# Kernel optimization log

Measured on AMD Instinct MI355X. Metric: run time of the kernel, lower is better.

The kernel has to match this reference:

```python
import jax, jax.numpy as jnp
import numpy as np

B, L, E, S = 4, 1024, 256, 32  # batch, seq_len, e_dim, local window half-size
NEG = -1e30  # stands in for excluding out-of-range positions from softmax


def setup_inputs() -> dict:
    key = jax.random.key(0)
    ks = jax.random.split(key, 8)
    sc = 1.0 / np.sqrt(E)
    return {
        "q": jax.random.normal(ks[0], (B, L, E), jnp.float32),
        "Wq": jax.random.normal(ks[1], (E, E), jnp.float32) * sc,
        "bq": jax.random.normal(ks[2], (E,), jnp.float32) * sc,
        "Wk": jax.random.normal(ks[3], (E, E), jnp.float32) * sc,
        "bk": jax.random.normal(ks[4], (E,), jnp.float32) * sc,
        "Wv": jax.random.normal(ks[5], (E, E), jnp.float32) * sc,
        "bv": jax.random.normal(ks[6], (E,), jnp.float32) * sc,
        "pos_bias": jax.random.normal(ks[7], (2 * S + 1, E), jnp.float32),
    }


def reference(q, Wq, bq, Wk, bk, Wv, bv, pos_bias):
    # Linear projections (nn.Linear: x @ W.T + b)
    Q = q @ Wq.T + bq
    K = q @ Wk.T + bk
    V = q @ Wv.T + bv

    W = 2 * S + 1
    rel = jnp.arange(-S, S + 1)                      # [W] relative offsets
    idx = jnp.arange(L)[:, None] + rel[None, :]       # [L, W] absolute positions
    valid = (idx >= 0) & (idx < L)                    # in-sequence window entries
    idxc = jnp.clip(idx, 0, L - 1)
    strict = jnp.abs(rel) < S                         # |j-i| < s mask (zeroes K at edges)

    # Gather windows: [B, L, W, E]
    K_win = K[:, idxc] + pos_bias[rel + S][None, None, :, :]
    K_masked = jnp.where(strict[None, None, :, None], K_win, 0.0)
    # Out-of-range positions excluded from softmax entirely (logit -> -inf)
    logits = jnp.where(valid[None, :, :, None], Q[:, :, None, :] * K_masked, NEG)
    weights = jax.nn.softmax(logits, axis=2)          # per-channel softmax over window

    V_win = jnp.where(valid[None, :, :, None], V[:, idxc], 0.0)
    ctx = jnp.sum(weights * V_win, axis=2)            # [B, L, E]

    sig = jax.nn.sigmoid(Q)
    # sigmoid applied inside the loop and again at the end -> squared
    return sig * sig * ctx
```

## Files before the change

kernel.cpp:

```cpp
#include <hip/hip_runtime.h>
#include <hip/hip_bf16.h>

#define B_ 4
#define L_ 1024
#define E_ 256
#define S_ 32

typedef __bf16 bf16x8 __attribute__((ext_vector_type(8)));
typedef float f32x4 __attribute__((ext_vector_type(4)));

__device__ __forceinline__ __bf16 bf_from_bits(unsigned short u) {
    __bf16 b;
    __builtin_memcpy(&b, &u, 2);
    return b;
}

__device__ __forceinline__ void split1(float x, unsigned short& h, unsigned short& l) {
    const unsigned u  = __float_as_uint(x);
    const unsigned hb = u & 0xFFFF0000u;
    h = (unsigned short)(hb >> 16);
    __bf16 lo = (__bf16)(x - __uint_as_float(hb));
    unsigned short lu;
    __builtin_memcpy(&lu, &lo, 2);
    l = lu;
}

__device__ __forceinline__ void load8split(const float* __restrict__ p,
                                           bf16x8& h, bf16x8& l) {
    const float4 x0 = *(const float4*)p;
    const float4 x1 = *(const float4*)(p + 4);
    const float xs[8] = {x0.x, x0.y, x0.z, x0.w, x1.x, x1.y, x1.z, x1.w};
#pragma unroll
    for (int j = 0; j < 8; ++j) {
        const unsigned hb = __float_as_uint(xs[j]) & 0xFFFF0000u;
        h[j] = bf_from_bits((unsigned short)(__float_as_uint(xs[j]) >> 16));
        l[j] = (__bf16)(xs[j] - __uint_as_float(hb));
    }
}

__global__ __launch_bounds__(256) void presplit(
    const float* __restrict__ A,
    const float* __restrict__ Wq, const float* __restrict__ Wk,
    const float* __restrict__ Wv,
    unsigned short* __restrict__ Ah, unsigned short* __restrict__ Al,
    unsigned short* __restrict__ Wh, unsigned short* __restrict__ Wl)
{
    const int e8 = (blockIdx.x * 256 + threadIdx.x) * 8;
    const float* src;
    unsigned short* dh;
    unsigned short* dl;
    if (e8 < 1048576) {
        src = A + e8; dh = Ah + e8; dl = Al + e8;
    } else {
        const int r = e8 - 1048576;
        const int m = r >> 16;
        const int o = r & 65535;
        src = (m == 0 ? Wq : m == 1 ? Wk : Wv) + o;
        dh = Wh + r; dl = Wl + r;
    }
    const float4 x0 = *(const float4*)src;
    const float4 x1 = *(const float4*)(src + 4);
    const float xs[8] = {x0.x, x0.y, x0.z, x0.w, x1.x, x1.y, x1.z, x1.w};
    unsigned short hs[8], ls[8];
#pragma unroll
    for (int j = 0; j < 8; ++j) split1(xs[j], hs[j], ls[j]);
    *(ushort4*)(dh)     = make_ushort4(hs[0], hs[1], hs[2], hs[3]);
    *(ushort4*)(dh + 4) = make_ushort4(hs[4], hs[5], hs[6], hs[7]);
    *(ushort4*)(dl)     = make_ushort4(ls[0], ls[1], ls[2], ls[3]);
    *(ushort4*)(dl + 4) = make_ushort4(ls[4], ls[5], ls[6], ls[7]);
}

__global__ __launch_bounds__(256, 2) void qkv_gemm3(
    const unsigned short* __restrict__ Ah, const unsigned short* __restrict__ Al,
    const unsigned short* __restrict__ Wh, const unsigned short* __restrict__ Wl,
    const float* __restrict__ bq, const float* __restrict__ bk,
    const float* __restrict__ bv,
    float* __restrict__ Qo, float* __restrict__ Ko, float* __restrict__ Vo)
{
    const int z = blockIdx.z;
    const float* bm = (z == 0) ? bq : (z == 1) ? bk : bv;
    float* Om       = (z == 0) ? Qo : (z == 1) ? Ko : Vo;
    const unsigned short* Whz = Wh + (size_t)z * 65536;
    const unsigned short* Wlz = Wl + (size_t)z * 65536;

    const int wave = threadIdx.x >> 6;
    const int lane = threadIdx.x & 63;
    const int rsel = lane & 15;
    const int koff = (lane >> 4) * 8;

    const int m0 = blockIdx.x * 32;
    const int nb = wave * 64;

    const unsigned short* pa0h = Ah + (size_t)(m0 + rsel) * 256 + koff;
    const unsigned short* pa0l = Al + (size_t)(m0 + rsel) * 256 + koff;
    const unsigned short* pa1h = pa0h + 16 * 256;
    const unsigned short* pa1l = pa0l + 16 * 256;

    const unsigned short* pwh[4];
    const unsigned short* pwl[4];
#pragma unroll
    for (int nt = 0; nt < 4; ++nt) {
        const size_t off = (size_t)(nb + nt * 16 + rsel) * 256 + koff;
        pwh[nt] = Whz + off;
        pwl[nt] = Wlz + off;
    }

    f32x4 acc[2][4];
#pragma unroll
    for (int mt = 0; mt < 2; ++mt)
#pragma unroll
        for (int nt = 0; nt < 4; ++nt)
            acc[mt][nt] = (f32x4){0.f, 0.f, 0.f, 0.f};

#pragma unroll
    for (int k0 = 0; k0 < 256; k0 += 32) {
        bf16x8 ah[2], al[2], bh[4], bl[4];
        ah[0] = *(const bf16x8*)(pa0h + k0);
        al[0] = *(const bf16x8*)(pa0l + k0);
        ah[1] = *(const bf16x8*)(pa1h + k0);
        al[1] = *(const bf16x8*)(pa1l + k0);
#pragma unroll
        for (int nt = 0; nt < 4; ++nt) {
            bh[nt] = *(const bf16x8*)(pwh[nt] + k0);
            bl[nt] = *(const bf16x8*)(pwl[nt] + k0);
        }
#pragma unroll
        for (int mt = 0; mt < 2; ++mt)
#pragma unroll
            for (int nt = 0; nt < 4; ++nt) {
                acc[mt][nt] = __builtin_amdgcn_mfma_f32_16x16x32_bf16(
                    ah[mt], bh[nt], acc[mt][nt], 0, 0, 0);
                acc[mt][nt] = __builtin_amdgcn_mfma_f32_16x16x32_bf16(
                    ah[mt], bl[nt], acc[mt][nt], 0, 0, 0);
                acc[mt][nt] = __builtin_amdgcn_mfma_f32_16x16x32_bf16(
                    al[mt], bh[nt], acc[mt][nt], 0, 0, 0);
            }
    }

#pragma unroll
    for (int mt = 0; mt < 2; ++mt) {
        const int mrow = m0 + mt * 16 + (lane >> 4) * 4;
#pragma unroll
        for (int nt = 0; nt < 4; ++nt) {
            const int n = nb + nt * 16 + rsel;
            const float bias = bm[n];
#pragma unroll
            for (int r = 0; r < 4; ++r)
                Om[(size_t)(mrow + r) * 256 + n] = acc[mt][nt][r] + bias;
        }
    }
}

#define TI2 32
#define CH2 64
#define HB2 96
#define PS2 68
#define LOG2E 1.4426950408889634f

__global__ __launch_bounds__(256) void aft_stage2c(
    const float* __restrict__ Q, const float* __restrict__ K,
    const float* __restrict__ V, const float* __restrict__ pb,
    float* __restrict__ out)
{
    __shared__ float Kw[HB2][PS2];
    __shared__ float Vw[HB2][PS2];
    __shared__ float Pw[2 * S_ + 1][PS2];

    const int tid = threadIdx.x;
    const int b  = blockIdx.y;
    const int i0 = blockIdx.x * TI2;
    const int c0 = blockIdx.z * CH2;

    const float* Kb = K + (size_t)b * L_ * E_;
    const float* Vb = V + (size_t)b * L_ * E_;

    for (int idx = tid; idx < HB2 * 16; idx += 256) {
        const int r  = idx >> 4;
        const int cq = (idx & 15) * 4;
        int j = i0 - S_ + r;
        j = j < 0 ? 0 : (j > L_ - 1 ? L_ - 1 : j);
        const size_t g = (size_t)j * E_ + c0 + cq;
        *(float4*)&Kw[r][cq] = *(const float4*)(Kb + g);
        *(float4*)&Vw[r][cq] = *(const float4*)(Vb + g);
    }
    for (int idx = tid; idx < (2 * S_ + 1) * 16; idx += 256) {
        const int r  = idx >> 4;
        const int cq = (idx & 15) * 4;
        *(float4*)&Pw[r][cq] = *(const float4*)(pb + (size_t)r * E_ + c0 + cq);
    }
    __syncthreads();

    const int cq = (tid & 15) * 4;
    const int t  = tid >> 4;
    const int i1 = i0 + 2 * t;
    const int i2 = i1 + 1;
    const int r0 = 2 * t;

    const float4 qa = *(const float4*)(Q + ((size_t)b * L_ + i1) * E_ + c0 + cq);
    const float4 qb2 = *(const float4*)(Q + ((size_t)b * L_ + i2) * E_ + c0 + cq);
    const float4 q2a = make_float4(qa.x * LOG2E, qa.y * LOG2E, qa.z * LOG2E, qa.w * LOG2E);
    const float4 q2b = make_float4(qb2.x * LOG2E, qb2.y * LOG2E, qb2.z * LOG2E, qb2.w * LOG2E);

    float4 den1 = {0, 0, 0, 0}, num1 = {0, 0, 0, 0};
    float4 den2 = {0, 0, 0, 0}, num2 = {0, 0, 0, 0};

    const bool interior = (blockIdx.x >= 1) && (blockIdx.x <= (L_ / TI2) - 2);

    if (interior) {
        {
            const float4 v = *(const float4*)&Vw[r0][cq];
            den1.x += 1.f; den1.y += 1.f; den1.z += 1.f; den1.w += 1.f;
            num1.x += v.x; num1.y += v.y; num1.z += v.z; num1.w += v.w;
        }
        float4 p_old;
        {
            const float4 p = *(const float4*)&Pw[1][cq];
            const float4 k = *(const float4*)&Kw[r0 + 1][cq];
            const float4 v = *(const float4*)&Vw[r0 + 1][cq];
            const float e0 = __builtin_amdgcn_exp2f(q2a.x * (k.x + p.x));
            const float e1 = __builtin_amdgcn_exp2f(q2a.y * (k.y + p.y));
            const float e2 = __builtin_amdgcn_exp2f(q2a.z * (k.z + p.z));
            const float e3 = __builtin_amdgcn_exp2f(q2a.w * (k.w + p.w));
            den1.x += e0; den1.y += e1; den1.z += e2; den1.w += e3;
            num1.x += e0 * v.x; num1.y += e1 * v.y; num1.z += e2 * v.z; num1.w += e3 * v.w;
            den2.x += 1.f; den2.y += 1.f; den2.z += 1.f; den2.w += 1.f;
            num2.x += v.x; num2.y += v.y; num2.z += v.z; num2.w += v.w;
            p_old = p;
        }
        for (int w1 = 2; w1 <= 63; ++w1) {
            const float4 p = *(const float4*)&Pw[w1][cq];
            const float4 k = *(const float4*)&Kw[r0 + w1][cq];
            const float4 v = *(const float4*)&Vw[r0 + w1][cq];
            const float a0 = __builtin_amdgcn_exp2f(q2a.x * (k.x + p.x));
            const float a1 = __builtin_amdgcn_exp2f(q2a.y * (k.y + p.y));
            const float a2 = __builtin_amdgcn_exp2f(q2a.z * (k.z + p.z));
            const float a3 = __builtin_amdgcn_exp2f(q2a.w * (k.w + p.w));
            const float b0 = __builtin_amdgcn_exp2f(q2b.x * (k.x + p_old.x));
            const float b1 = __builtin_amdgcn_exp2f(q2b.y * (k.y + p_old.y));
            const float b2 = __builtin_amdgcn_exp2f(q2b.z * (k.z + p_old.z));
            const float b3 = __builtin_amdgcn_exp2f(q2b.w * (k.w + p_old.w));
            den1.x += a0; den1.y += a1; den1.z += a2; den1.w += a3;
            num1.x += a0 * v.x; num1.y += a1 * v.y; num1.z += a2 * v.z; num1.w += a3 * v.w;
            den2.x += b0; den2.y += b1; den2.z += b2; den2.w += b3;
            num2.x += b0 * v.x; num2.y += b1 * v.y; num2.z += b2 * v.z; num2.w += b3 * v.w;
            p_old = p;
        }
        {
            const float4 k = *(const float4*)&Kw[r0 + 64][cq];
            const float4 v = *(const float4*)&Vw[r0 + 64][cq];
            den1.x += 1.f; den1.y += 1.f; den1.z += 1.f; den1.w += 1.f;
            num1.x += v.x; num1.y += v.y; num1.z += v.z; num1.w += v.w;
            const float b0 = __builtin_amdgcn_exp2f(q2b.x * (k.x + p_old.x));
            const float b1 = __builtin_amdgcn_exp2f(q2b.y * (k.y + p_old.y));
            const float b2 = __builtin_amdgcn_exp2f(q2b.z * (k.z + p_old.z));
            const float b3 = __builtin_amdgcn_exp2f(q2b.w * (k.w + p_old.w));
            den2.x += b0; den2.y += b1; den2.z += b2; den2.w += b3;
            num2.x += b0 * v.x; num2.y += b1 * v.y; num2.z += b2 * v.z; num2.w += b3 * v.w;
        }
        {
            const float4 v = *(const float4*)&Vw[r0 + 65][cq];
            den2.x += 1.f; den2.y += 1.f; den2.z += 1.f; den2.w += 1.f;
            num2.x += v.x; num2.y += v.y; num2.z += v.z; num2.w += v.w;
        }
    } else {
#pragma unroll
        for (int rowsel = 0; rowsel < 2; ++rowsel) {
            const int i = rowsel ? i2 : i1;
            const float4 q2 = rowsel ? q2b : q2a;
            float4* den = rowsel ? &den2 : &den1;
            float4* num = rowsel ? &num2 : &num1;
            for (int w = 0; w <= 64; ++w) {
                const int j = i - S_ + w;
                const bool valid = (unsigned)j < (unsigned)L_;
                const int r = (i - i0) + w;
                const float4 k = *(const float4*)&Kw[r][cq];
                const float4 v = *(const float4*)&Vw[r][cq];
                const float4 p = *(const float4*)&Pw[w][cq];
                const bool edge = (w == 0) || (w == 64);
                const float lx = edge ? 0.f : q2.x * (k.x + p.x);
                const float ly = edge ? 0.f : q2.y * (k.y + p.y);
                const float lz = edge ? 0.f : q2.z * (k.z + p.z);
                const float lw = edge ? 0.f : q2.w * (k.w + p.w);
                const float e0 = valid ? __builtin_amdgcn_exp2f(lx) : 0.f;
                const float e1 = valid ? __builtin_amdgcn_exp2f(ly) : 0.f;
                const float e2 = valid ? __builtin_amdgcn_exp2f(lz) : 0.f;
                const float e3 = valid ? __builtin_amdgcn_exp2f(lw) : 0.f;
                den->x += e0; den->y += e1; den->z += e2; den->w += e3;
                num->x += e0 * v.x; num->y += e1 * v.y;
                num->z += e2 * v.z; num->w += e3 * v.w;
            }
        }
    }

    {
        const float s0 = 1.f / (1.f + __builtin_amdgcn_exp2f(-q2a.x));
        const float s1 = 1.f / (1.f + __builtin_amdgcn_exp2f(-q2a.y));
        const float s2 = 1.f / (1.f + __builtin_amdgcn_exp2f(-q2a.z));
        const float s3 = 1.f / (1.f + __builtin_amdgcn_exp2f(-q2a.w));
        float4 o;
        o.x = s0 * s0 * num1.x / den1.x;
        o.y = s1 * s1 * num1.y / den1.y;
        o.z = s2 * s2 * num1.z / den1.z;
        o.w = s3 * s3 * num1.w / den1.w;
        *(float4*)(out + ((size_t)b * L_ + i1) * E_ + c0 + cq) = o;
    }
    {
        const float s0 = 1.f / (1.f + __builtin_amdgcn_exp2f(-q2b.x));
        const float s1 = 1.f / (1.f + __builtin_amdgcn_exp2f(-q2b.y));
        const float s2 = 1.f / (1.f + __builtin_amdgcn_exp2f(-q2b.z));
        const float s3 = 1.f / (1.f + __builtin_amdgcn_exp2f(-q2b.w));
        float4 o;
        o.x = s0 * s0 * num2.x / den2.x;
        o.y = s1 * s1 * num2.y / den2.y;
        o.z = s2 * s2 * num2.z / den2.z;
        o.w = s3 * s3 * num2.w / den2.w;
        *(float4*)(out + ((size_t)b * L_ + i2) * E_ + c0 + cq) = o;
    }
}

#define TI 32
#define CG 64
#define RK 96
#define LDP 68

__global__ __launch_bounds__(256) void aft_fused(
    const float* __restrict__ q,
    const float* __restrict__ Wq, const float* __restrict__ bq,
    const float* __restrict__ Wk, const float* __restrict__ bk,
    const float* __restrict__ Wv, const float* __restrict__ bv,
    const float* __restrict__ pb,
    float* __restrict__ out)
{
    __shared__ float Kl[RK][LDP];
    __shared__ float Vl[RK][LDP];
    __shared__ float Ql[TI][LDP];

    const int i0 = blockIdx.x * TI;
    const int b  = blockIdx.y;
    const int c0 = blockIdx.z * CG;

    const int wave = threadIdx.x >> 6;
    const int lane = threadIdx.x & 63;
    const int rsel = lane & 15;
    const int koff = (lane >> 4) * 8;

    const float* qb = q + (size_t)b * L_ * E_;

    for (int job = wave; job < 56; job += 4) {
        int p, rt, ct;
        if (job < 24)      { p = 0; rt = job >> 2;        ct = job & 3; }
        else if (job < 48) { p = 1; rt = (job - 24) >> 2; ct = (job - 24) & 3; }
        else               { p = 2; rt = (job - 48) >> 2; ct = (job - 48) & 3; }

        int jrow = (p == 2) ? (i0 + rt * 16 + rsel)
                            : (i0 - S_ + rt * 16 + rsel);
        int jc = jrow < 0 ? 0 : (jrow > L_ - 1 ? L_ - 1 : jrow);
        const float* pa = qb + (size_t)jc * E_ + koff;

        const float* Wm = (p == 0) ? Wk : (p == 1) ? Wv : Wq;
        const float* bm = (p == 0) ? bk : (p == 1) ? bv : bq;
        const int n = c0 + ct * 16 + rsel;
        const float* pw = Wm + (size_t)n * E_ + koff;

        f32x4 acc = {0.f, 0.f, 0.f, 0.f};
#pragma unroll
        for (int k0 = 0; k0 < 256; k0 += 32) {
            bf16x8 ah, al, bh, bl;
            load8split(pa + k0, ah, al);
            load8split(pw + k0, bh, bl);
            acc = __builtin_amdgcn_mfma_f32_16x16x32_bf16(ah, bh, acc, 0, 0, 0);
            acc = __builtin_amdgcn_mfma_f32_16x16x32_bf16(ah, bl, acc, 0, 0, 0);
            acc = __builtin_amdgcn_mfma_f32_16x16x32_bf16(al, bh, acc, 0, 0, 0);
        }

        const float bias = bm[n];
        const int row0 = rt * 16 + (lane >> 4) * 4;
        const int colc = ct * 16 + rsel;
        float* dst = (p == 0) ? &Kl[0][0] : (p == 1) ? &Vl[0][0] : &Ql[0][0];
#pragma unroll
        for (int r = 0; r < 4; ++r)
            dst[(size_t)(row0 + r) * LDP + colc] = acc[r] + bias;
    }
    __syncthreads();

    const int cq  = threadIdx.x & 15;
    const int is0 = threadIdx.x >> 4;
    const int cL  = cq * 4;
    const int cG  = c0 + cL;
    const float* pbc = pb + cG;

    for (int rr = is0; rr < TI; rr += 16) {
        const int i = i0 + rr;
        const float4 qv = *(const float4*)&Ql[rr][cL];

        float den0 = 0.f, den1 = 0.f, den2 = 0.f, den3 = 0.f;
        float num0 = 0.f, num1 = 0.f, num2 = 0.f, num3 = 0.f;

        const int jlo = (i - S_ < 0) ? 0 : (i - S_);
        const int jhi = (i + S_ > L_ - 1) ? (L_ - 1) : (i + S_);

        for (int j = jlo; j <= jhi; ++j) {
            const int r = j - (i0 - S_);
            const int w = j - i + S_;
            const float4 vv = *(const float4*)&Vl[r][cL];

            float kx = 0.f, ky = 0.f, kz = 0.f, kw = 0.f;
            if (w != 0 && w != 2 * S_) {
                const float4 kk = *(const float4*)&Kl[r][cL];
                const float4 pp = *(const float4*)(pbc + (size_t)w * E_);
                kx = kk.x + pp.x;
                ky = kk.y + pp.y;
                kz = kk.z + pp.z;
                kw = kk.w + pp.w;
            }
            const float e0 = __expf(qv.x * kx);
            const float e1 = __expf(qv.y * ky);
            const float e2 = __expf(qv.z * kz);
            const float e3 = __expf(qv.w * kw);
            den0 += e0; den1 += e1; den2 += e2; den3 += e3;
            num0 += e0 * vv.x; num1 += e1 * vv.y;
            num2 += e2 * vv.z; num3 += e3 * vv.w;
        }

        const float s0 = 1.f / (1.f + __expf(-qv.x));
        const float s1 = 1.f / (1.f + __expf(-qv.y));
        const float s2 = 1.f / (1.f + __expf(-qv.z));
        const float s3 = 1.f / (1.f + __expf(-qv.w));

        float4 o;
        o.x = s0 * s0 * num0 / den0;
        o.y = s1 * s1 * num1 / den1;
        o.z = s2 * s2 * num2 / den2;
        o.w = s3 * s3 * num3 / den3;
        *(float4*)(out + ((size_t)b * L_ + i) * E_ + cG) = o;
    }
}

extern "C" void kernel_launch(void* const* d_in, const int* in_sizes, int n_in,
                              void* d_out, int out_size, void* d_ws, size_t ws_size,
                              hipStream_t stream) {
    const float* q  = (const float*)d_in[0];
    const float* Wq = (const float*)d_in[1];
    const float* bq = (const float*)d_in[2];
    const float* Wk = (const float*)d_in[3];
    const float* bk = (const float*)d_in[4];
    const float* Wv = (const float*)d_in[5];
    const float* bv = (const float*)d_in[6];
    const float* pb = (const float*)d_in[7];

    const size_t needA = (size_t)3 * 1048576 * 4 + (size_t)2 * 1048576 * 2
                       + (size_t)2 * 196608 * 2;

    if (ws_size >= needA) {
        float* Qf = (float*)d_ws;
        float* Kf = Qf + 1048576;
        float* Vf = Kf + 1048576;
        unsigned short* Ah = (unsigned short*)(Vf + 1048576);
        unsigned short* Al = Ah + 1048576;
        unsigned short* Wh = Al + 1048576;
        unsigned short* Wl = Wh + 196608;

        presplit<<<dim3(608), 256, 0, stream>>>(q, Wq, Wk, Wv, Ah, Al, Wh, Wl);
        qkv_gemm3<<<dim3(128, 1, 3), 256, 0, stream>>>(Ah, Al, Wh, Wl,
                                                       bq, bk, bv, Qf, Kf, Vf);
        aft_stage2c<<<dim3(L_ / TI2, B_, E_ / CH2), 256, 0, stream>>>(
            Qf, Kf, Vf, pb, (float*)d_out);
    } else {
        aft_fused<<<dim3(L_ / TI, B_, E_ / CG), 256, 0, stream>>>(
            q, Wq, bq, Wk, bk, Wv, bv, pb, (float*)d_out);
    }
}
```

Baseline: 126.7 us.

## Fuse QKV projection GEMM into local-window attention kernel via shared memory

Result: slower. 145.5 us (+14.9%).

```diff
diff --git a/kernel.cpp b/kernel.cpp
--- a/kernel.cpp
+++ b/kernel.cpp
@@ -70,123 +70,81 @@
     *(ushort4*)(dl + 4) = make_ushort4(ls[4], ls[5], ls[6], ls[7]);
 }
 
-__global__ __launch_bounds__(256, 2) void qkv_gemm3(
+#define PS2 68
+#define LOG2E 1.4426950408889634f
+
+__global__ __launch_bounds__(256, 2) void aft_fused2(
     const unsigned short* __restrict__ Ah, const unsigned short* __restrict__ Al,
     const unsigned short* __restrict__ Wh, const unsigned short* __restrict__ Wl,
     const float* __restrict__ bq, const float* __restrict__ bk,
-    const float* __restrict__ bv,
-    float* __restrict__ Qo, float* __restrict__ Ko, float* __restrict__ Vo)
+    const float* __restrict__ bv, const float* __restrict__ pb,
+    float* __restrict__ out)
 {
-    const int z = blockIdx.z;
-    const float* bm = (z == 0) ? bq : (z == 1) ? bk : bv;
-    float* Om       = (z == 0) ? Qo : (z == 1) ? Ko : Vo;
-    const unsigned short* Whz = Wh + (size_t)z * 65536;
-    const unsigned short* Wlz = Wl + (size_t)z * 65536;
-
-    const int wave = threadIdx.x >> 6;
-    const int lane = threadIdx.x & 63;
+    __shared__ float Kw[96][PS2];
+    __shared__ float Vw[96][PS2];
+    __shared__ float Qw[32][PS2];
+    __shared__ float Pw[2 * S_ + 1][PS2];
+
+    const int tid = threadIdx.x;
+    const int i0 = blockIdx.x * 32;
+    const int b  = blockIdx.y;
+    const int c0 = blockIdx.z * 64;
+
+    for (int idx = tid; idx < (2 * S_ + 1) * 16; idx += 256) {
+        const int r  = idx >> 4;
+        const int cc = (idx & 15) * 4;
+        *(float4*)&Pw[r][cc] = *(const float4*)(pb + (size_t)r * E_ + c0 + cc);
+    }
+
+    const int wave = tid >> 6;
+    const int lane = tid & 63;
     const int rsel = lane & 15;
     const int koff = (lane >> 4) * 8;
 
-    const int m0 = blockIdx.x * 32;
-    const int nb = wave * 64;
-
-    const unsigned short* pa0h = Ah + (size_t)(m0 + rsel) * 256 + koff;
-    const unsigned short* pa0l = Al + (size_t)(m0 + rsel) * 256 + koff;
-    const unsigned short* pa1h = pa0h + 16 * 256;
-    const unsigned short* pa1l = pa0l + 16 * 256;
-
-    const unsigned short* pwh[4];
-    const unsigned short* pwl[4];
-#pragma unroll
-    for (int nt = 0; nt < 4; ++nt) {
-        const size_t off = (size_t)(nb + nt * 16 + rsel) * 256 + koff;
-        pwh[nt] = Whz + off;
-        pwl[nt] = Wlz + off;
-    }
-
-    f32x4 acc[2][4];
-#pragma unroll
-    for (int mt = 0; mt < 2; ++mt)
-#pragma unroll
-        for (int nt = 0; nt < 4; ++nt)
-            acc[mt][nt] = (f32x4){0.f, 0.f, 0.f, 0.f};
-
-#pragma unroll
-    for (int k0 = 0; k0 < 256; k0 += 32) {
-        bf16x8 ah[2], al[2], bh[4], bl[4];
-        ah[0] = *(const bf16x8*)(pa0h + k0);
-        al[0] = *(const bf16x8*)(pa0l + k0);
-        ah[1] = *(const bf16x8*)(pa1h + k0);
-        al[1] = *(const bf16x8*)(pa1l + k0);
-#pragma unroll
-        for (int nt = 0; nt < 4; ++nt) {
-            bh[nt] = *(const bf16x8*)(pwh[nt] + k0);
-            bl[nt] = *(const bf16x8*)(pwl[nt] + k0);
-        }
-#pragma unroll
-        for (int mt = 0; mt < 2; ++mt)
-#pragma unroll
-            for (int nt = 0; nt < 4; ++nt) {
-                acc[mt][nt] = __builtin_amdgcn_mfma_f32_16x16x32_bf16(
-                    ah[mt], bh[nt], acc[mt][nt], 0, 0, 0);
-                acc[mt][nt] = __builtin_amdgcn_mfma_f32_16x16x32_bf16(
-                    ah[mt], bl[nt], acc[mt][nt], 0, 0, 0);
-                acc[mt][nt] = __builtin_amdgcn_mfma_f32_16x16x32_bf16(
-                    al[mt], bh[nt], acc[mt][nt], 0, 0, 0);
+    const int ct = wave;
+    const int n  = c0 + ct * 16 + rsel;
+    const int colc = ct * 16 + rsel;
+    const int crow = (lane >> 4) * 4;
+
+#pragma unroll
+    for (int p = 0; p < 3; ++p) {
+        const int z = (p == 0) ? 1 : (p == 1) ? 2 : 0;
+        const float bias = (p == 0) ? bk[n] : (p == 1) ? bv[n] : bq[n];
+        float* dst = (p == 0) ? &Kw[0][0] : (p == 1) ? &Vw[0][0] : &Qw[0][0];
+        const int nrt = (p == 2) ? 2 : 6;
+
+        const unsigned short* wh = Wh + (size_t)z * 65536 + (size_t)n * 256 + koff;
+        const unsigned short* wl = Wl + (size_t)z * 65536 + (size_t)n * 256 + koff;
+        bf16x8 BH[8], BL[8];
+#pragma unroll
+        for (int s = 0; s < 8; ++s) {
+            BH[s] = *(const bf16x8*)(wh + s * 32);
+            BL[s] = *(const bf16x8*)(wl + s * 32);
+        }
+
+        for (int rt = 0; rt < nrt; ++rt) {
+            int arow = (p == 2) ? (i0 + rt * 16 + rsel)
+                                : (i0 - S_ + rt * 16 + rsel);
+            arow = arow < 0 ? 0 : (arow > L_ - 1 ? L_ - 1 : arow);
+            const size_t abase = ((size_t)b * L_ + arow) * 256 + koff;
+            const unsigned short* pah = Ah + abase;
+            const unsigned short* pal = Al + abase;
+
+            f32x4 acc = {0.f, 0.f, 0.f, 0.f};
+#pragma unroll
+            for (int s = 0; s < 8; ++s) {
+                const bf16x8 ah = *(const bf16x8*)(pah + s * 32);
+                const bf16x8 al = *(const bf16x8*)(pal + s * 32);
+                acc = __builtin_amdgcn_mfma_f32_16x16x32_bf16(ah, BH[s], acc, 0, 0, 0);
+                acc = __builtin_amdgcn_mfma_f32_16x16x32_bf16(ah, BL[s], acc, 0, 0, 0);
+                acc = __builtin_amdgcn_mfma_f32_16x16x32_bf16(al, BH[s], acc, 0, 0, 0);
             }
-    }
-
-#pragma unroll
-    for (int mt = 0; mt < 2; ++mt) {
-        const int mrow = m0 + mt * 16 + (lane >> 4) * 4;
-#pragma unroll
-        for (int nt = 0; nt < 4; ++nt) {
-            const int n = nb + nt * 16 + rsel;
-            const float bias = bm[n];
+
+            const int row0 = rt * 16 + crow;
 #pragma unroll
             for (int r = 0; r < 4; ++r)
-                Om[(size_t)(mrow + r) * 256 + n] = acc[mt][nt][r] + bias;
-        }
-    }
-}
-
-#define TI2 32
-#define CH2 64
-#define HB2 96
-#define PS2 68
-#define LOG2E 1.4426950408889634f
-
-__global__ __launch_bounds__(256) void aft_stage2c(
-    const float* __restrict__ Q, const float* __restrict__ K,
-    const float* __restrict__ V, const float* __restrict__ pb,
-    float* __restrict__ out)
-{
-    __shared__ float Kw[HB2][PS2];
-    __shared__ float Vw[HB2][PS2];
-    __shared__ float Pw[2 * S_ + 1][PS2];
-
-    const int tid = threadIdx.x;
-    const int b  = blockIdx.y;
-    const int i0 = blockIdx.x * TI2;
-    const int c0 = blockIdx.z * CH2;
-
-    const float* Kb = K + (size_t)b * L_ * E_;
-    const float* Vb = V + (size_t)b * L_ * E_;
-
-    for (int idx = tid; idx < HB2 * 16; idx += 256) {
-        const int r  = idx >> 4;
-        const int cq = (idx & 15) * 4;
-        int j = i0 - S_ + r;
-        j = j < 0 ? 0 : (j > L_ - 1 ? L_ - 1 : j);
-        const size_t g = (size_t)j * E_ + c0 + cq;
-        *(float4*)&Kw[r][cq] = *(const float4*)(Kb + g);
-        *(float4*)&Vw[r][cq] = *(const float4*)(Vb + g);
-    }
-    for (int idx = tid; idx < (2 * S_ + 1) * 16; idx += 256) {
-        const int r  = idx >> 4;
-        const int cq = (idx & 15) * 4;
-        *(float4*)&Pw[r][cq] = *(const float4*)(pb + (size_t)r * E_ + c0 + cq);
+                dst[(size_t)(row0 + r) * PS2 + colc] = acc[r] + bias;
+        }
     }
     __syncthreads();
 
@@ -196,15 +154,15 @@
     const int i2 = i1 + 1;
     const int r0 = 2 * t;
 
-    const float4 qa = *(const float4*)(Q + ((size_t)b * L_ + i1) * E_ + c0 + cq);
-    const float4 qb2 = *(const float4*)(Q + ((size_t)b * L_ + i2) * E_ + c0 + cq);
+    const float4 qa  = *(const float4*)&Qw[2 * t][cq];
+    const float4 qb2 = *(const float4*)&Qw[2 * t + 1][cq];
     const float4 q2a = make_float4(qa.x * LOG2E, qa.y * LOG2E, qa.z * LOG2E, qa.w * LOG2E);
     const float4 q2b = make_float4(qb2.x * LOG2E, qb2.y * LOG2E, qb2.z * LOG2E, qb2.w * LOG2E);
 
     float4 den1 = {0, 0, 0, 0}, num1 = {0, 0, 0, 0};
     float4 den2 = {0, 0, 0, 0}, num2 = {0, 0, 0, 0};
 
-    const bool interior = (blockIdx.x >= 1) && (blockIdx.x <= (L_ / TI2) - 2);
+    const bool interior = (blockIdx.x >= 1) && (blockIdx.x <= (L_ / 32) - 2);
 
     if (interior) {
         {
@@ -448,23 +406,17 @@
     const float* bv = (const float*)d_in[6];
     const float* pb = (const float*)d_in[7];
 
-    const size_t needA = (size_t)3 * 1048576 * 4 + (size_t)2 * 1048576 * 2
-                       + (size_t)2 * 196608 * 2;
+    const size_t needA = ((size_t)2 * 1048576 + (size_t)2 * 196608) * 2;
 
     if (ws_size >= needA) {
-        float* Qf = (float*)d_ws;
-        float* Kf = Qf + 1048576;
-        float* Vf = Kf + 1048576;
-        unsigned short* Ah = (unsigned short*)(Vf + 1048576);
+        unsigned short* Ah = (unsigned short*)d_ws;
         unsigned short* Al = Ah + 1048576;
         unsigned short* Wh = Al + 1048576;
         unsigned short* Wl = Wh + 196608;
 
         presplit<<<dim3(608), 256, 0, stream>>>(q, Wq, Wk, Wv, Ah, Al, Wh, Wl);
-        qkv_gemm3<<<dim3(128, 1, 3), 256, 0, stream>>>(Ah, Al, Wh, Wl,
-                                                       bq, bk, bv, Qf, Kf, Vf);
-        aft_stage2c<<<dim3(L_ / TI2, B_, E_ / CH2), 256, 0, stream>>>(
-            Qf, Kf, Vf, pb, (float*)d_out);
+        aft_fused2<<<dim3(L_ / 32, B_, E_ / 64), 256, 0, stream>>>(
+            Ah, Al, Wh, Wl, bq, bk, bv, pb, (float*)d_out);
     } else {
         aft_fused<<<dim3(L_ / TI, B_, E_ / CG), 256, 0, stream>>>(
             q, Wq, bq, Wk, bk, Wv, bv, pb, (float*)d_out);
```

## Split QKV GEMM across N and stream K/V windows from global memory

Applied to the files above, without the earlier changes.

Result: no change. 126.5 us (-0.1%).

```diff
diff --git a/kernel.cpp b/kernel.cpp
--- a/kernel.cpp
+++ b/kernel.cpp
@@ -5,6 +5,7 @@
 #define L_ 1024
 #define E_ 256
 #define S_ 32
+#define LOG2E 1.4426950408889634f
 
 typedef __bf16 bf16x8 __attribute__((ext_vector_type(8)));
 typedef float f32x4 __attribute__((ext_vector_type(4)));
@@ -70,7 +71,7 @@
     *(ushort4*)(dl + 4) = make_ushort4(ls[4], ls[5], ls[6], ls[7]);
 }
 
-__global__ __launch_bounds__(256, 2) void qkv_gemm3(
+__global__ __launch_bounds__(256) void qkv_gemm4(
     const unsigned short* __restrict__ Ah, const unsigned short* __restrict__ Al,
     const unsigned short* __restrict__ Wh, const unsigned short* __restrict__ Wl,
     const float* __restrict__ bq, const float* __restrict__ bk,
@@ -89,45 +90,39 @@
     const int koff = (lane >> 4) * 8;
 
     const int m0 = blockIdx.x * 32;
-    const int nb = wave * 64;
+    const int nb = blockIdx.y * 128 + wave * 32;
 
     const unsigned short* pa0h = Ah + (size_t)(m0 + rsel) * 256 + koff;
     const unsigned short* pa0l = Al + (size_t)(m0 + rsel) * 256 + koff;
     const unsigned short* pa1h = pa0h + 16 * 256;
     const unsigned short* pa1l = pa0l + 16 * 256;
-
-    const unsigned short* pwh[4];
-    const unsigned short* pwl[4];
-#pragma unroll
-    for (int nt = 0; nt < 4; ++nt) {
-        const size_t off = (size_t)(nb + nt * 16 + rsel) * 256 + koff;
-        pwh[nt] = Whz + off;
-        pwl[nt] = Wlz + off;
-    }
-
-    f32x4 acc[2][4];
+    const unsigned short* pw0h = Whz + (size_t)(nb + rsel) * 256 + koff;
+    const unsigned short* pw0l = Wlz + (size_t)(nb + rsel) * 256 + koff;
+    const unsigned short* pw1h = pw0h + 16 * 256;
+    const unsigned short* pw1l = pw0l + 16 * 256;
+
+    f32x4 acc[2][2];
 #pragma unroll
     for (int mt = 0; mt < 2; ++mt)
 #pragma unroll
-        for (int nt = 0; nt < 4; ++nt)
+        for (int nt = 0; nt < 2; ++nt)
             acc[mt][nt] = (f32x4){0.f, 0.f, 0.f, 0.f};
 
 #pragma unroll
     for (int k0 = 0; k0 < 256; k0 += 32) {
-        bf16x8 ah[2], al[2], bh[4], bl[4];
+        bf16x8 ah[2], al[2], bh[2], bl[2];
         ah[0] = *(const bf16x8*)(pa0h + k0);
         al[0] = *(const bf16x8*)(pa0l + k0);
         ah[1] = *(const bf16x8*)(pa1h + k0);
         al[1] = *(const bf16x8*)(pa1l + k0);
-#pragma unroll
-        for (int nt = 0; nt < 4; ++nt) {
-            bh[nt] = *(const bf16x8*)(pwh[nt] + k0);
-            bl[nt] = *(const bf16x8*)(pwl[nt] + k0);
-        }
+        bh[0] = *(const bf16x8*)(pw0h + k0);
+        bl[0] = *(const bf16x8*)(pw0l + k0);
+        bh[1] = *(const bf16x8*)(pw1h + k0);
+        bl[1] = *(const bf16x8*)(pw1l + k0);
 #pragma unroll
         for (int mt = 0; mt < 2; ++mt)
 #pragma unroll
-            for (int nt = 0; nt < 4; ++nt) {
+            for (int nt = 0; nt < 2; ++nt) {
                 acc[mt][nt] = __builtin_amdgcn_mfma_f32_16x16x32_bf16(
                     ah[mt], bh[nt], acc[mt][nt], 0, 0, 0);
                 acc[mt][nt] = __builtin_amdgcn_mfma_f32_16x16x32_bf16(
@@ -141,7 +136,7 @@
     for (int mt = 0; mt < 2; ++mt) {
         const int mrow = m0 + mt * 16 + (lane >> 4) * 4;
 #pragma unroll
-        for (int nt = 0; nt < 4; ++nt) {
+        for (int nt = 0; nt < 2; ++nt) {
             const int n = nb + nt * 16 + rsel;
             const float bias = bm[n];
 #pragma unroll
@@ -151,171 +146,102 @@
     }
 }
 
-#define TI2 32
-#define CH2 64
-#define HB2 96
-#define PS2 68
-#define LOG2E 1.4426950408889634f
-
-__global__ __launch_bounds__(256) void aft_stage2c(
+#define SPS 36
+
+__global__ __launch_bounds__(256, 4) void aft_stage3(
     const float* __restrict__ Q, const float* __restrict__ K,
     const float* __restrict__ V, const float* __restrict__ pb,
     float* __restrict__ out)
 {
-    __shared__ float Kw[HB2][PS2];
-    __shared__ float Vw[HB2][PS2];
-    __shared__ float Pw[2 * S_ + 1][PS2];
+    __shared__ float Pw[2 * S_ + 1][SPS];
 
     const int tid = threadIdx.x;
+    const int i0 = blockIdx.x * 32;
     const int b  = blockIdx.y;
-    const int i0 = blockIdx.x * TI2;
-    const int c0 = blockIdx.z * CH2;
-
-    const float* Kb = K + (size_t)b * L_ * E_;
-    const float* Vb = V + (size_t)b * L_ * E_;
-
-    for (int idx = tid; idx < HB2 * 16; idx += 256) {
-        const int r  = idx >> 4;
-        const int cq = (idx & 15) * 4;
-        int j = i0 - S_ + r;
-        j = j < 0 ? 0 : (j > L_ - 1 ? L_ - 1 : j);
-        const size_t g = (size_t)j * E_ + c0 + cq;
-        *(float4*)&Kw[r][cq] = *(const float4*)(Kb + g);
-        *(float4*)&Vw[r][cq] = *(const float4*)(Vb + g);
-    }
-    for (int idx = tid; idx < (2 * S_ + 1) * 16; idx += 256) {
-        const int r  = idx >> 4;
-        const int cq = (idx & 15) * 4;
-        *(float4*)&Pw[r][cq] = *(const float4*)(pb + (size_t)r * E_ + c0 + cq);
+    const int c0 = blockIdx.z * 32;
+
+    for (int idx = tid; idx < 65 * 8; idx += 256) {
+        const int r = idx >> 3;
+        const int q = (idx & 7) * 4;
+        *(float4*)&Pw[r][q] = *(const float4*)(pb + (size_t)r * E_ + c0 + q);
     }
     __syncthreads();
 
-    const int cq = (tid & 15) * 4;
-    const int t  = tid >> 4;
-    const int i1 = i0 + 2 * t;
-    const int i2 = i1 + 1;
-    const int r0 = 2 * t;
-
-    const float4 qa = *(const float4*)(Q + ((size_t)b * L_ + i1) * E_ + c0 + cq);
-    const float4 qb2 = *(const float4*)(Q + ((size_t)b * L_ + i2) * E_ + c0 + cq);
-    const float4 q2a = make_float4(qa.x * LOG2E, qa.y * LOG2E, qa.z * LOG2E, qa.w * LOG2E);
-    const float4 q2b = make_float4(qb2.x * LOG2E, qb2.y * LOG2E, qb2.z * LOG2E, qb2.w * LOG2E);
-
-    float4 den1 = {0, 0, 0, 0}, num1 = {0, 0, 0, 0};
-    float4 den2 = {0, 0, 0, 0}, num2 = {0, 0, 0, 0};
-
-    const bool interior = (blockIdx.x >= 1) && (blockIdx.x <= (L_ / TI2) - 2);
+    const int c4 = (tid & 7) * 4;
+    const int ro = tid >> 3;
+    const int i  = i0 + ro;
+
+    const float4 qv = *(const float4*)(Q + ((size_t)b * L_ + i) * E_ + c0 + c4);
+    const float q2x = qv.x * LOG2E, q2y = qv.y * LOG2E;
+    const float q2z = qv.z * LOG2E, q2w = qv.w * LOG2E;
+
+    float den0 = 0.f, den1 = 0.f, den2 = 0.f, den3 = 0.f;
+    float num0 = 0.f, num1 = 0.f, num2 = 0.f, num3 = 0.f;
+
+    const float* kp = K + ((size_t)b * L_ + (i - S_)) * E_ + c0 + c4;
+    const float* vp = V + ((size_t)b * L_ + (i - S_)) * E_ + c0 + c4;
+
+    const bool interior = (blockIdx.x >= 1) && (blockIdx.x <= 30);
 
     if (interior) {
         {
-            const float4 v = *(const float4*)&Vw[r0][cq];
-            den1.x += 1.f; den1.y += 1.f; den1.z += 1.f; den1.w += 1.f;
-            num1.x += v.x; num1.y += v.y; num1.z += v.z; num1.w += v.w;
-        }
-        float4 p_old;
+            const float4 v = *(const float4*)vp;
+            den0 += 1.f; den1 += 1.f; den2 += 1.f; den3 += 1.f;
+            num0 += v.x; num1 += v.y; num2 += v.z; num3 += v.w;
+        }
+#pragma unroll 7
+        for (int w = 1; w <= 63; ++w) {
+            const float4 kk = *(const float4*)(kp + (size_t)w * E_);
+            const float4 vv = *(const float4*)(vp + (size_t)w * E_);
+            const float4 pp = *(const float4*)&Pw[w][c4];
+            const float e0 = __builtin_amdgcn_exp2f(q2x * (kk.x + pp.x));
+            const float e1 = __builtin_amdgcn_exp2f(q2y * (kk.y + pp.y));
+            const float e2 = __builtin_amdgcn_exp2f(q2z * (kk.z + pp.z));
+            const float e3 = __builtin_amdgcn_exp2f(q2w * (kk.w + pp.w));
+            den0 += e0; den1 += e1; den2 += e2; den3 += e3;
+            num0 += e0 * vv.x; num1 += e1 * vv.y;
+            num2 += e2 * vv.z; num3 += e3 * vv.w;
+        }
         {
-            const float4 p = *(const float4*)&Pw[1][cq];
-            const float4 k = *(const float4*)&Kw[r0 + 1][cq];
-            const float4 v = *(const float4*)&Vw[r0 + 1][cq];
-            const float e0 = __builtin_amdgcn_exp2f(q2a.x * (k.x + p.x));
-            const float e1 = __builtin_amdgcn_exp2f(q2a.y * (k.y + p.y));
-            const float e2 = __builtin_amdgcn_exp2f(q2a.z * (k.z + p.z));
-            const float e3 = __builtin_amdgcn_exp2f(q2a.w * (k.w + p.w));
-            den1.x += e0; den1.y += e1; den1.z += e2; den1.w += e3;
-            num1.x += e0 * v.x; num1.y += e1 * v.y; num1.z += e2 * v.z; num1.w += e3 * v.w;
-            den2.x += 1.f; den2.y += 1.f; den2.z += 1.f; den2.w += 1.f;
-            num2.x += v.x; num2.y += v.y; num2.z += v.z; num2.w += v.w;
-            p_old = p;
-        }
-        for (int w1 = 2; w1 <= 63; ++w1) {
-            const float4 p = *(const float4*)&Pw[w1][cq];
-            const float4 k = *(const float4*)&Kw[r0 + w1][cq];
-            const float4 v = *(const float4*)&Vw[r0 + w1][cq];
-            const float a0 = __builtin_amdgcn_exp2f(q2a.x * (k.x + p.x));
-            const float a1 = __builtin_amdgcn_exp2f(q2a.y * (k.y + p.y));
-            const float a2 = __builtin_amdgcn_exp2f(q2a.z * (k.z + p.z));
-            const float a3 = __builtin_amdgcn_exp2f(q2a.w * (k.w + p.w));
-            const float b0 = __builtin_amdgcn_exp2f(q2b.x * (k.x + p_old.x));
-            const float b1 = __builtin_amdgcn_exp2f(q2b.y * (k.y + p_old.y));
-            const float b2 = __builtin_amdgcn_exp2f(q2b.z * (k.z + p_old.z));
-            const float b3 = __builtin_amdgcn_exp2f(q2b.w * (k.w + p_old.w));
-            den1.x += a0; den1.y += a1; den1.z += a2; den1.w += a3;
-            num1.x += a0 * v.x; num1.y += a1 * v.y; num1.z += a2 * v.z; num1.w += a3 * v.w;
-            den2.x += b0; den2.y += b1; den2.z += b2; den2.w += b3;
-            num2.x += b0 * v.x; num2.y += b1 * v.y; num2.z += b2 * v.z; num2.w += b3 * v.w;
-            p_old = p;
-        }
-        {
-            const float4 k = *(const float4*)&Kw[r0 + 64][cq];
-            const float4 v = *(const float4*)&Vw[r0 + 64][cq];
-            den1.x += 1.f; den1.y += 1.f; den1.z += 1.f; den1.w += 1.f;
-            num1.x += v.x; num1.y += v.y; num1.z += v.z; num1.w += v.w;
-            const float b0 = __builtin_amdgcn_exp2f(q2b.x * (k.x + p_old.x));
-            const float b1 = __builtin_amdgcn_exp2f(q2b.y * (k.y + p_old.y));
-            const float b2 = __builtin_amdgcn_exp2f(q2b.z * (k.z + p_old.z));
-            const float b3 = __builtin_amdgcn_exp2f(q2b.w * (k.w + p_old.w));
-            den2.x += b0; den2.y += b1; den2.z += b2; den2.w += b3;
-            num2.x += b0 * v.x; num2.y += b1 * v.y; num2.z += b2 * v.z; num2.w += b3 * v.w;
-        }
-        {
-            const float4 v = *(const float4*)&Vw[r0 + 65][cq];
-            den2.x += 1.f; den2.y += 1.f; den2.z += 1.f; den2.w += 1.f;
-            num2.x += v.x; num2.y += v.y; num2.z += v.z; num2.w += v.w;
+            const float4 v = *(const float4*)(vp + (size_t)64 * E_);
+            den0 += 1.f; den1 += 1.f; den2 += 1.f; den3 += 1.f;
+            num0 += v.x; num1 += v.y; num2 += v.z; num3 += v.w;
         }
     } else {
-#pragma unroll
-        for (int rowsel = 0; rowsel < 2; ++rowsel) {
-            const int i = rowsel ? i2 : i1;
-            const float4 q2 = rowsel ? q2b : q2a;
-            float4* den = rowsel ? &den2 : &den1;
-            float4* num = rowsel ? &num2 : &num1;
-            for (int w = 0; w <= 64; ++w) {
-                const int j = i - S_ + w;
-                const bool valid = (unsigned)j < (unsigned)L_;
-                const int r = (i - i0) + w;
-                const float4 k = *(const float4*)&Kw[r][cq];
-                const float4 v = *(const float4*)&Vw[r][cq];
-                const float4 p = *(const float4*)&Pw[w][cq];
-                const bool edge = (w == 0) || (w == 64);
-                const float lx = edge ? 0.f : q2.x * (k.x + p.x);
-                const float ly = edge ? 0.f : q2.y * (k.y + p.y);
-                const float lz = edge ? 0.f : q2.z * (k.z + p.z);
-                const float lw = edge ? 0.f : q2.w * (k.w + p.w);
-                const float e0 = valid ? __builtin_amdgcn_exp2f(lx) : 0.f;
-                const float e1 = valid ? __builtin_amdgcn_exp2f(ly) : 0.f;
-                const float e2 = valid ? __builtin_amdgcn_exp2f(lz) : 0.f;
-                const float e3 = valid ? __builtin_amdgcn_exp2f(lw) : 0.f;
-                den->x += e0; den->y += e1; den->z += e2; den->w += e3;
-                num->x += e0 * v.x; num->y += e1 * v.y;
-                num->z += e2 * v.z; num->w += e3 * v.w;
-            }
-        }
-    }
-
-    {
-        const float s0 = 1.f / (1.f + __builtin_amdgcn_exp2f(-q2a.x));
-        const float s1 = 1.f / (1.f + __builtin_amdgcn_exp2f(-q2a.y));
-        const float s2 = 1.f / (1.f + __builtin_amdgcn_exp2f(-q2a.z));
-        const float s3 = 1.f / (1.f + __builtin_amdgcn_exp2f(-q2a.w));
-        float4 o;
-        o.x = s0 * s0 * num1.x / den1.x;
-        o.y = s1 * s1 * num1.y / den1.y;
-        o.z = s2 * s2 * num1.z / den1.z;
-        o.w = s3 * s3 * num1.w / den1.w;
-        *(float4*)(out + ((size_t)b * L_ + i1) * E_ + c0 + cq) = o;
-    }
-    {
-        const float s0 = 1.f / (1.f + __builtin_amdgcn_exp2f(-q2b.x));
-        const float s1 = 1.f / (1.f + __builtin_amdgcn_exp2f(-q2b.y));
-        const float s2 = 1.f / (1.f + __builtin_amdgcn_exp2f(-q2b.z));
-        const float s3 = 1.f / (1.f + __builtin_amdgcn_exp2f(-q2b.w));
-        float4 o;
-        o.x = s0 * s0 * num2.x / den2.x;
-        o.y = s1 * s1 * num2.y / den2.y;
-        o.z = s2 * s2 * num2.z / den2.z;
-        o.w = s3 * s3 * num2.w / den2.w;
-        *(float4*)(out + ((size_t)b * L_ + i2) * E_ + c0 + cq) = o;
-    }
+        const float* KbB = K + (size_t)b * L_ * E_ + c0 + c4;
+        const float* VbB = V + (size_t)b * L_ * E_ + c0 + c4;
+        for (int w = 0; w <= 64; ++w) {
+            const int j = i - S_ + w;
+            const bool valid = (unsigned)j < (unsigned)L_;
+            const int jc = j < 0 ? 0 : (j > L_ - 1 ? L_ - 1 : j);
+            const float4 kk = *(const float4*)(KbB + (size_t)jc * E_);
+            const float4 vv = *(const float4*)(VbB + (size_t)jc * E_);
+            const float4 pp = *(const float4*)&Pw[w][c4];
+            const bool edge = (w == 0) || (w == 64);
+            const float lx = edge ? 0.f : q2x * (kk.x + pp.x);
+            const float ly = edge ? 0.f : q2y * (kk.y + pp.y);
+            const float lz = edge ? 0.f : q2z * (kk.z + pp.z);
+            const float lw = edge ? 0.f : q2w * (kk.w + pp.w);
+            const float e0 = valid ? __builtin_amdgcn_exp2f(lx) : 0.f;
+            const float e1 = valid ? __builtin_amdgcn_exp2f(ly) : 0.f;
+            const float e2 = valid ? __builtin_amdgcn_exp2f(lz) : 0.f;
+            const float e3 = valid ? __builtin_amdgcn_exp2f(lw) : 0.f;
+            den0 += e0; den1 += e1; den2 += e2; den3 += e3;
+            num0 += e0 * vv.x; num1 += e1 * vv.y;
+            num2 += e2 * vv.z; num3 += e3 * vv.w;
+        }
+    }
+
+    const float s0 = 1.f / (1.f + __builtin_amdgcn_exp2f(-q2x));
+    const float s1 = 1.f / (1.f + __builtin_amdgcn_exp2f(-q2y));
+    const float s2 = 1.f / (1.f + __builtin_amdgcn_exp2f(-q2z));
+    const float s3 = 1.f / (1.f + __builtin_amdgcn_exp2f(-q2w));
+    float4 o;
+    o.x = s0 * s0 * num0 / den0;
+    o.y = s1 * s1 * num1 / den1;
+    o.z = s2 * s2 * num2 / den2;
+    o.w = s3 * s3 * num3 / den3;
+    *(float4*)(out + ((size_t)b * L_ + i) * E_ + c0 + c4) = o;
 }
 
 #define TI 32
@@ -448,8 +374,8 @@
     const float* bv = (const float*)d_in[6];
     const float* pb = (const float*)d_in[7];
 
-    const size_t needA = (size_t)3 * 1048576 * 4 + (size_t)2 * 1048576 * 2
-                       + (size_t)2 * 196608 * 2;
+    const size_t needA = (size_t)3 * 1048576 * 4
+                       + ((size_t)2 * 1048576 + (size_t)2 * 196608) * 2;
 
     if (ws_size >= needA) {
         float* Qf = (float*)d_ws;
@@ -461,10 +387,10 @@
         unsigned short* Wl = Wh + 196608;
 
         presplit<<<dim3(608), 256, 0, stream>>>(q, Wq, Wk, Wv, Ah, Al, Wh, Wl);
-        qkv_gemm3<<<dim3(128, 1, 3), 256, 0, stream>>>(Ah, Al, Wh, Wl,
+        qkv_gemm4<<<dim3(128, 2, 3), 256, 0, stream>>>(Ah, Al, Wh, Wl,
                                                        bq, bk, bv, Qf, Kf, Vf);
-        aft_stage2c<<<dim3(L_ / TI2, B_, E_ / CH2), 256, 0, stream>>>(
-            Qf, Kf, Vf, pb, (float*)d_out);
+        aft_stage3<<<dim3(32, 4, 8), 256, 0, stream>>>(Qf, Kf, Vf, pb,
+                                                       (float*)d_out);
     } else {
         aft_fused<<<dim3(L_ / TI, B_, E_ / CG), 256, 0, stream>>>(
             q, Wq, bq, Wk, bk, Wv, bv, pb, (float*)d_out);
```
